# Kernel optimization log

Hardware: AMD Instinct MI355X
Metric: run time of the kernel (lower is better)

Reference implementation:

```python
import jax, jax.numpy as jnp
import numpy as np

N = 100_000   # nodes
E = 3_200_000 # edges (avg degree 32)
F_NODE = 64
F_EDGE = 16
HID = 64
NEG_SLOPE = 0.2


def _gat_conv(x, src, dst, edge_attr, W, a_src, a_dst, We, a_e, bias, n):
    """PyG GATConv (heads=1, edge_dim, add_self_loops=True fill='mean', eval mode)."""
    # --- add self loops; loop edge_attr = mean of incoming edge_attr per node ---
    deg = jax.ops.segment_sum(jnp.ones((src.shape[0],), x.dtype), dst, num_segments=n)
    loop_attr = jax.ops.segment_sum(edge_attr, dst, num_segments=n)
    loop_attr = jnp.where(deg[:, None] > 0, loop_attr / jnp.maximum(deg, 1.0)[:, None], 0.0)
    loop = jnp.arange(n, dtype=src.dtype)
    src2 = jnp.concatenate([src, loop])
    dst2 = jnp.concatenate([dst, loop])
    ea = jnp.concatenate([edge_attr, loop_attr], axis=0)

    # --- node / edge projections and per-node attention terms ---
    h = x @ W                                   # [N, HID]
    alpha_src = h @ a_src                       # [N]
    alpha_dst = h @ a_dst                       # [N]
    e = ea @ We                                 # [E+N, HID]
    alpha_e = e @ a_e                           # [E+N]

    # --- per-edge logits + segment softmax over destination neighborhoods ---
    logits = jax.nn.leaky_relu(alpha_src[src2] + alpha_dst[dst2] + alpha_e, NEG_SLOPE)
    seg_max = jax.ops.segment_max(logits, dst2, num_segments=n)  # every node has self loop
    ex = jnp.exp(logits - seg_max[dst2])
    denom = jax.ops.segment_sum(ex, dst2, num_segments=n)
    w = ex / denom[dst2]                        # [E+N]

    # --- weighted scatter-aggregate of messages ---
    out = jax.ops.segment_sum(h[src2] * w[:, None], dst2, num_segments=n)
    return out + bias


def setup_inputs() -> dict:
    key = jax.random.key(0)
    ks = jax.random.split(key, 16)
    s = 0.1  # keep logits tame
    return {
        "x": jax.random.normal(ks[0], (N, F_NODE), jnp.float32),
        "edge_index": jax.random.randint(ks[1], (2, E), 0, N, jnp.int32),
        "edge_attr": jax.random.normal(ks[2], (E, F_EDGE), jnp.float32),
        "W1": jax.random.normal(ks[3], (F_NODE, HID), jnp.float32) * s,
        "att_src1": jax.random.normal(ks[4], (HID,), jnp.float32) * s,
        "att_dst1": jax.random.normal(ks[5], (HID,), jnp.float32) * s,
        "We1": jax.random.normal(ks[6], (F_EDGE, HID), jnp.float32) * s,
        "att_edge1": jax.random.normal(ks[7], (HID,), jnp.float32) * s,
        "b1": jnp.zeros((HID,), jnp.float32),
        "W2": jax.random.normal(ks[8], (HID, HID), jnp.float32) * s,
        "att_src2": jax.random.normal(ks[9], (HID,), jnp.float32) * s,
        "att_dst2": jax.random.normal(ks[10], (HID,), jnp.float32) * s,
        "We2": jax.random.normal(ks[11], (F_EDGE, HID), jnp.float32) * s,
        "att_edge2": jax.random.normal(ks[12], (HID,), jnp.float32) * s,
        "b2": jnp.zeros((HID,), jnp.float32),
        "fc_w": jax.random.normal(ks[13], (HID, 1), jnp.float32) * s,
        "fc_b": jnp.zeros((1,), jnp.float32),
    }


def reference(x, edge_index, edge_attr, W1, att_src1, att_dst1, We1, att_edge1, b1,
              W2, att_src2, att_dst2, We2, att_edge2, b2, fc_w, fc_b):
    src, dst = edge_index[0], edge_index[1]
    n = x.shape[0]
    h = jax.nn.elu(_gat_conv(x, src, dst, edge_attr, W1, att_src1, att_dst1, We1, att_edge1, b1, n))
    h = jax.nn.elu(_gat_conv(h, src, dst, edge_attr, W2, att_src2, att_dst2, We2, att_edge2, b2, n))
    return h @ fc_w + fc_b  # [N, 1] logits
```

## Files before the change

kernel.cpp:

```cpp
#include <hip/hip_runtime.h>
#include <hip/hip_bf16.h>
#include <hip/hip_fp16.h>
#include <math.h>
#include <stdint.h>

constexpr int HIDDIM = 64;
constexpr int FEDGE  = 16;
constexpr int BN     = 512;
constexpr int CAP    = 17000;
constexpr int TILE   = 4096;
constexpr int NTA    = 512;
constexpr int EPT    = TILE / NTA;
constexpr int GBLK   = 1536;

__global__ void compute_c_kernel(const float* __restrict__ We1, const float* __restrict__ ae1,
                                 const float* __restrict__ We2, const float* __restrict__ ae2,
                                 float* __restrict__ c, int* __restrict__ bucketCursor) {
  int t = threadIdx.x;
  if (t < 512) bucketCursor[t] = 0;
  if (t < FEDGE) {
    float s = 0.f;
    for (int j = 0; j < HIDDIM; ++j) s += We1[t * HIDDIM + j] * ae1[j];
    c[t] = s;
  } else if (t < 2 * FEDGE) {
    int k = t - FEDGE;
    float s = 0.f;
    for (int j = 0; j < HIDDIM; ++j) s += We2[k * HIDDIM + j] * ae2[j];
    c[FEDGE + k] = s;
  }
}

__device__ __forceinline__ int pack_ae(float a1, float a2) {
  unsigned lo = __half_as_ushort(__float2half_rn(a1));
  unsigned hi = __half_as_ushort(__float2half_rn(a2));
  return (int)((hi << 16) | lo);
}
template <int SEL>
__device__ __forceinline__ float unpack_ae(int pk) {
  unsigned u = (SEL == 0) ? ((unsigned)pk & 0xFFFFu) : ((unsigned)pk >> 16);
  return __half2float(__ushort_as_half((unsigned short)u));
}

__global__ __launch_bounds__(NTA) void passA_gemm_kernel(
    const int* __restrict__ src, const int* __restrict__ dst,
    const float* __restrict__ attr, const float* __restrict__ c,
    int* __restrict__ bucketCursor, int2* __restrict__ P, int E, int nbuck, int ablocks,
    const float* __restrict__ X, const float* __restrict__ W,
    const float* __restrict__ a_src, const float* __restrict__ a_dst,
    __half2* __restrict__ H, float* __restrict__ alpha_s, float* __restrict__ alpha_d, int N) {
  __shared__ char smem[57856];
  int t = threadIdx.x;

  if (blockIdx.x < ablocks) {
    int*  st_ae = (int*)smem;
    int*  s_key = st_ae + TILE;
    int*  s_ae  = s_key + TILE;
    unsigned char* s_b = (unsigned char*)(s_ae + TILE);
    int*  cnt   = (int*)(s_b + TILE);
    int*  lbase = cnt + 256;
    int*  gbase = lbase + 512;
    int*  wsum  = gbase + 256;
    float* cs   = (float*)(wsum + 8);

    if (t < 32) cs[t] = c[t];
    if (t < nbuck) cnt[t] = 0;
    __syncthreads();
    int e0 = blockIdx.x * TILE;
    int tileCnt = min(TILE, E - e0);

    int d_reg[EPT];
#pragma unroll
    for (int k = 0; k < EPT; ++k) {
      int e = e0 + k * NTA + t;
      d_reg[k] = (e < E) ? dst[e] : -1;
    }
#pragma unroll
    for (int k = 0; k < EPT; ++k) {
      if (d_reg[k] >= 0) atomicAdd(&cnt[d_reg[k] >> 9], 1);
    }
    __syncthreads();

    int lane = t & 63, w = t >> 6;
    int n = (t < nbuck) ? cnt[t] : 0;
    int ret = 0;
    if (n > 0) ret = atomicAdd(&bucketCursor[t], n);
    int incl = n;
#pragma unroll
    for (int d = 1; d < 64; d <<= 1) {
      int tv = __shfl_up(incl, d, 64);
      if (lane >= d) incl += tv;
    }
    if (lane == 63) wsum[w] = incl;
    __syncthreads();
    {
      int woff = 0;
#pragma unroll
      for (int w2 = 0; w2 < 8; ++w2) woff += (w2 < w) ? wsum[w2] : 0;
      lbase[t] = incl - n + woff;
      if (t < nbuck) { gbase[t] = ret; cnt[t] = 0; }
    }

    {
      int q   = t & 3;
      int grp = t >> 2;
      const float4* attr4 = (const float4*)attr;
#pragma unroll
      for (int pass = 0; pass < TILE / 128; ++pass) {
        int el = pass * 128 + grp;
        int e = e0 + el;
        float4 v = make_float4(0.f, 0.f, 0.f, 0.f);
        if (e < E) v = attr4[(size_t)e * 4 + q];
        float a1 = v.x * cs[4*q]    + v.y * cs[4*q+1]    + v.z * cs[4*q+2]    + v.w * cs[4*q+3];
        float a2 = v.x * cs[16+4*q] + v.y * cs[16+4*q+1] + v.z * cs[16+4*q+2] + v.w * cs[16+4*q+3];
        a1 += __shfl_xor(a1, 1, 64); a1 += __shfl_xor(a1, 2, 64);
        a2 += __shfl_xor(a2, 1, 64); a2 += __shfl_xor(a2, 2, 64);
        if (q == 0) st_ae[el] = pack_ae(a1, a2);
      }
    }
    __syncthreads();

#pragma unroll
    for (int k = 0; k < EPT; ++k) {
      int d = d_reg[k];
      if (d < 0) continue;
      int el = k * NTA + t;
      int e = e0 + el;
      int b = d >> 9;
      int sE = src[e];
      int r = atomicAdd(&cnt[b], 1);
      int idx = lbase[b] + r;
      s_key[idx] = sE | ((d & 511) << 20);
      s_ae[idx]  = st_ae[el];
      s_b[idx]   = (unsigned char)b;
    }
    __syncthreads();

    for (int i = t; i < tileCnt; i += NTA) {
      int b = s_b[i];
      int rank = i - lbase[b];
      int pos = gbase[b] + rank;
      if (pos < CAP) P[(size_t)b * CAP + pos] = make_int2(s_key[i], s_ae[i]);
    }
  } else {
    float* Ws   = (float*)smem;
    float* as_s = Ws + HIDDIM * HIDDIM;
    float* ad_s = as_s + HIDDIM;
    for (int i = t; i < HIDDIM * HIDDIM; i += NTA) Ws[i] = W[i];
    if (t < HIDDIM) {
      as_s[t] = a_src[t];
      ad_s[t] = a_dst[t];
    }
    __syncthreads();
    int lane = t & 63;
    int wid  = t >> 6;
    int gbid = blockIdx.x - ablocks;
    int wavesTotal = 8 * GBLK;
    for (int row = gbid * 8 + wid; row < N; row += wavesTotal) {
      float xv = X[(size_t)row * HIDDIM + lane];
      float acc = 0.f;
#pragma unroll
      for (int k = 0; k < HIDDIM; ++k) {
        float xk = __shfl(xv, k, 64);
        acc = fmaf(xk, Ws[k * HIDDIM + lane], acc);
      }
      float accN = __shfl_xor(acc, 1, 64);
      if (!(lane & 1)) {
        H[(size_t)row * 32 + (lane >> 1)] = __floats2half2_rn(acc, accN);
      }
      float s1 = acc * as_s[lane];
      float s2 = acc * ad_s[lane];
#pragma unroll
      for (int d = 32; d > 0; d >>= 1) {
        s1 += __shfl_xor(s1, d, 64);
        s2 += __shfl_xor(s2, d, 64);
      }
      if (lane == 0) {
        alpha_s[row] = s1;
        alpha_d[row] = s2;
      }
    }
  }
}

__global__ void scan_buckets_kernel(const int* __restrict__ bucketCursor,
                                    int* __restrict__ bucketBase,
                                    int* __restrict__ offsets, int nbuck, int N, int E) {
  __shared__ int s[512];
  int t = threadIdx.x;
  int v = (t < nbuck) ? min(bucketCursor[t], CAP) : 0;
  s[t] = v;
  __syncthreads();
  for (int d = 1; d < 512; d <<= 1) {
    int tv = (t >= d) ? s[t - d] : 0;
    __syncthreads();
    s[t] += tv;
    __syncthreads();
  }
  if (t < nbuck) bucketBase[t] = s[t] - v;
  if (t == 0) offsets[N] = E;
}

__global__ __launch_bounds__(512) void passB_kernel(
    const int2* __restrict__ P, const int* __restrict__ bucketCursor,
    const int* __restrict__ bucketBase, int* __restrict__ offsets,
    int2* __restrict__ EDGS, int N) {
  int b = blockIdx.x;
  int t = threadIdx.x;
  int nodeBase = b * BN;
  int cnt = min(bucketCursor[b], CAP);
  int gbase = bucketBase[b];
  __shared__ int hist[BN];
  __shared__ int cur[BN];
  __shared__ int wsum[8];
  hist[t] = 0;
  __syncthreads();
  const int2* Pb = P + (size_t)b * CAP;
  for (int i = t; i < cnt; i += 512) {
    int dl = (Pb[i].x >> 20) & 511;
    atomicAdd(&hist[dl], 1);
  }
  __syncthreads();
  int deg = hist[t];
  int lane = t & 63, w = t >> 6;
  int incl = deg;
#pragma unroll
  for (int d = 1; d < 64; d <<= 1) {
    int tv = __shfl_up(incl, d, 64);
    if (lane >= d) incl += tv;
  }
  if (lane == 63) wsum[w] = incl;
  __syncthreads();
  int woff = 0;
#pragma unroll
  for (int w2 = 0; w2 < 8; ++w2) woff += (w2 < w) ? wsum[w2] : 0;
  int excl = incl - deg + woff;
  int nodeId = nodeBase + t;
  if (nodeId < N) offsets[nodeId] = gbase + excl;
  cur[t] = gbase + excl;
  __syncthreads();
  for (int i = t; i < cnt; i += 512) {
    int2 r = Pb[i];
    int dl = (r.x >> 20) & 511;
    int pos = atomicAdd(&cur[dl], 1);
    EDGS[pos] = r;
  }
}

template <bool IN16>
__global__ __launch_bounds__(256) void gemm_alpha_kernel(
    const void* __restrict__ Xv, const float* __restrict__ W,
    const float* __restrict__ a_src, const float* __restrict__ a_dst,
    __half2* __restrict__ H, float* __restrict__ alpha_s, float* __restrict__ alpha_d, int n) {
  __shared__ float Ws[HIDDIM * HIDDIM];
  __shared__ float as_s[HIDDIM], ad_s[HIDDIM];
  for (int i = threadIdx.x; i < HIDDIM * HIDDIM; i += blockDim.x) Ws[i] = W[i];
  if (threadIdx.x < HIDDIM) {
    as_s[threadIdx.x] = a_src[threadIdx.x];
    ad_s[threadIdx.x] = a_dst[threadIdx.x];
  }
  __syncthreads();
  int lane = threadIdx.x & 63;
  int wid  = threadIdx.x >> 6;
  int wavesTotal = (blockDim.x >> 6) * gridDim.x;
  for (int row = blockIdx.x * (blockDim.x >> 6) + wid; row < n; row += wavesTotal) {
    float xv;
    if (IN16) xv = __half2float(((const __half*)Xv)[(size_t)row * HIDDIM + lane]);
    else      xv = ((const float*)Xv)[(size_t)row * HIDDIM + lane];
    float acc = 0.f;
#pragma unroll
    for (int k = 0; k < HIDDIM; ++k) {
      float xk = __shfl(xv, k, 64);
      acc = fmaf(xk, Ws[k * HIDDIM + lane], acc);
    }
    float accN = __shfl_xor(acc, 1, 64);
    if (!(lane & 1)) {
      H[(size_t)row * 32 + (lane >> 1)] = __floats2half2_rn(acc, accN);
    }
    float s1 = acc * as_s[lane];
    float s2 = acc * ad_s[lane];
#pragma unroll
    for (int d = 32; d > 0; d >>= 1) {
      s1 += __shfl_xor(s1, d, 64);
      s2 += __shfl_xor(s2, d, 64);
    }
    if (lane == 0) {
      alpha_s[row] = s1;
      alpha_d[row] = s2;
    }
  }
}

__device__ __forceinline__ float leaky(float x) { return (x < 0.f) ? 0.2f * x : x; }
__device__ __forceinline__ float elu(float x) { return (x > 0.f) ? x : (__expf(x) - 1.f); }

template <bool FINAL, int SEL>
__global__ __launch_bounds__(256) void aggregate_kernel(
    const __half2* __restrict__ H, const float* __restrict__ alpha_s, const float* __restrict__ alpha_d,
    const int2* __restrict__ EDGS, const int* __restrict__ offsets,
    const float* __restrict__ bias, const float* __restrict__ fc_w, const float* __restrict__ fc_b,
    void* __restrict__ out, int n) {
  int lane = threadIdx.x & 63;
  int wid  = threadIdx.x >> 6;
  int node = blockIdx.x * (blockDim.x >> 6) + wid;
  if (node >= n) return;
  int off = offsets[node];
  int deg = offsets[node + 1] - off;
  float ad  = alpha_d[node];
  float asn = alpha_s[node];

  if (deg <= 64) {
    int2 ed = make_int2(0, 0);
    if (lane < deg) ed = EDGS[off + lane];
    int   s_l  = ed.x & 0xFFFFF;
    float ae_l = unpack_ae<SEL>(ed.y);
    float as_g = (lane < deg) ? alpha_s[s_l] : 0.f;
    float lg_l = (lane < deg) ? leaky(as_g + ad + ae_l) : -INFINITY;
    float aesum = (lane < deg) ? ae_l : 0.f;
    float lmax = lg_l;
#pragma unroll
    for (int d = 32; d > 0; d >>= 1) {
      lmax = fmaxf(lmax, __shfl_xor(lmax, d, 64));
      aesum += __shfl_xor(aesum, d, 64);
    }
    float self_ae = (deg > 0) ? aesum / (float)deg : 0.f;
    float slg = leaky(asn + ad + self_ae);
    float m = fmaxf(lmax, slg);

    float ex_l = (lane < deg) ? __expf(lg_l - m) : 0.f;
    float dsum = ex_l;
#pragma unroll
    for (int d = 32; d > 0; d >>= 1) dsum += __shfl_xor(dsum, d, 64);
    float exs = __expf(slg - m);
    float denom = dsum + exs;

    int half = lane >> 5;
    int c32  = lane & 31;

    float selfw = (half == 0) ? exs : 0.f;
    float2 hv = __half22float2(H[(size_t)node * 32 + c32]);
    float2 acc2;
    acc2.x = selfw * hv.x;
    acc2.y = selfw * hv.y;

    int jj = 0;
    for (; jj + 16 <= deg; jj += 16) {
      int   si[8]; float ei[8];
#pragma unroll
      for (int k = 0; k < 8; ++k) {
        si[k] = __shfl(s_l, jj + 2 * k + half, 64);
        ei[k] = __shfl(ex_l, jj + 2 * k + half, 64);
      }
      float2 hh[8];
#pragma unroll
      for (int k = 0; k < 8; ++k) hh[k] = __half22float2(H[(size_t)si[k] * 32 + c32]);
#pragma unroll
      for (int k = 0; k < 8; ++k) {
        acc2.x = fmaf(ei[k], hh[k].x, acc2.x);
        acc2.y = fmaf(ei[k], hh[k].y, acc2.y);
      }
    }
    for (; jj + 8 <= deg; jj += 8) {
      int j0 = jj + half, j1 = jj + 2 + half, j2 = jj + 4 + half, j3 = jj + 6 + half;
      int   sa = __shfl(s_l, j0, 64),  sb = __shfl(s_l, j1, 64);
      int   sc = __shfl(s_l, j2, 64),  sd = __shfl(s_l, j3, 64);
      float ea = __shfl(ex_l, j0, 64), eb = __shfl(ex_l, j1, 64);
      float ec = __shfl(ex_l, j2, 64), ef = __shfl(ex_l, j3, 64);
      float2 ha = __half22float2(H[(size_t)sa * 32 + c32]);
      float2 hb = __half22float2(H[(size_t)sb * 32 + c32]);
      float2 hc = __half22float2(H[(size_t)sc * 32 + c32]);
      float2 hd = __half22float2(H[(size_t)sd * 32 + c32]);
      acc2.x = fmaf(ea, ha.x, acc2.x); acc2.y = fmaf(ea, ha.y, acc2.y);
      acc2.x = fmaf(eb, hb.x, acc2.x); acc2.y = fmaf(eb, hb.y, acc2.y);
      acc2.x = fmaf(ec, hc.x, acc2.x); acc2.y = fmaf(ec, hc.y, acc2.y);
      acc2.x = fmaf(ef, hd.x, acc2.x); acc2.y = fmaf(ef, hd.y, acc2.y);
    }
    for (; jj < deg; jj += 2) {
      int j = jj + half;
      int   sj = __shfl(s_l, j, 64);
      float ej = __shfl(ex_l, j, 64);
      float2 hj = __half22float2(H[(size_t)sj * 32 + c32]);
      acc2.x = fmaf(ej, hj.x, acc2.x);
      acc2.y = fmaf(ej, hj.y, acc2.y);
    }
    acc2.x += __shfl_xor(acc2.x, 32, 64);
    acc2.y += __shfl_xor(acc2.y, 32, 64);

    const float2* bi2 = (const float2*)bias;
    float2 bv = bi2[c32];
    float rx = elu(acc2.x / denom + bv.x);
    float ry = elu(acc2.y / denom + bv.y);
    if (!FINAL) {
      if (half == 0) {
        ((__half2*)out)[(size_t)node * 32 + c32] = __floats2half2_rn(rx, ry);
      }
    } else {
      const float2* fw2 = (const float2*)fc_w;
      float2 fv = fw2[c32];
      float s1 = rx * fv.x + ry * fv.y;
#pragma unroll
      for (int d = 16; d > 0; d >>= 1) s1 += __shfl_xor(s1, d, 64);
      if (lane == 0) ((float*)out)[node] = s1 + fc_b[0];
    }
    return;
  }

  {
    const __half* Hh = (const __half*)H;
    float lmax = -INFINITY, aesum = 0.f;
    for (int base = 0; base < deg; base += 64) {
      int i = base + lane;
      if (i < deg) {
        int2 ed = EDGS[off + i];
        int s = ed.x & 0xFFFFF;
        float ae = unpack_ae<SEL>(ed.y);
        float lg = leaky(alpha_s[s] + ad + ae);
        lmax = fmaxf(lmax, lg);
        aesum += ae;
      }
    }
#pragma unroll
    for (int d = 32; d > 0; d >>= 1) {
      lmax = fmaxf(lmax, __shfl_xor(lmax, d, 64));
      aesum += __shfl_xor(aesum, d, 64);
    }
    float self_ae = aesum / (float)deg;
    float slg = leaky(asn + ad + self_ae);
    float m = fmaxf(lmax, slg);
    float exs = __expf(slg - m);
    float dsum = 0.f;
    float acc = exs * __half2float(Hh[(size_t)node * HIDDIM + lane]);
    for (int base = 0; base < deg; base += 64) {
      int i = base + lane;
      int cnt = min(64, deg - base);
      int2 ed = make_int2(0, 0);
      if (i < deg) ed = EDGS[off + i];
      int   s_l  = ed.x & 0xFFFFF;
      float ae_l = unpack_ae<SEL>(ed.y);
      float ex_l = (lane < cnt) ? __expf(leaky(alpha_s[s_l] + ad + ae_l) - m) : 0.f;
      dsum += ex_l;
      for (int j = 0; j < cnt; ++j) {
        int   sj = __shfl(s_l, j, 64);
        float ej = __shfl(ex_l, j, 64);
        acc = fmaf(ej, __half2float(Hh[(size_t)sj * HIDDIM + lane]), acc);
      }
    }
#pragma unroll
    for (int d = 32; d > 0; d >>= 1) dsum += __shfl_xor(dsum, d, 64);
    float denom = dsum + exs;

    float res = elu(acc / denom + bias[lane]);
    if (!FINAL) {
      ((__half*)out)[(size_t)node * HIDDIM + lane] = __float2half_rn(res);
    } else {
      float s1 = res * fc_w[lane];
#pragma unroll
      for (int d = 32; d > 0; d >>= 1) s1 += __shfl_xor(s1, d, 64);
      if (lane == 0) ((float*)out)[node] = s1 + fc_b[0];
    }
  }
}

extern "C" void kernel_launch(void* const* d_in, const int* in_sizes, int n_in,
                              void* d_out, int out_size, void* d_ws, size_t ws_size,
                              hipStream_t stream) {
  const float* x    = (const float*)d_in[0];
  const int*   ei   = (const int*)d_in[1];
  const float* attr = (const float*)d_in[2];
  const float* W1   = (const float*)d_in[3];
  const float* as1  = (const float*)d_in[4];
  const float* ad1  = (const float*)d_in[5];
  const float* We1  = (const float*)d_in[6];
  const float* ae1  = (const float*)d_in[7];
  const float* b1   = (const float*)d_in[8];
  const float* W2   = (const float*)d_in[9];
  const float* as2  = (const float*)d_in[10];
  const float* ad2  = (const float*)d_in[11];
  const float* We2  = (const float*)d_in[12];
  const float* ae2  = (const float*)d_in[13];
  const float* b2   = (const float*)d_in[14];
  const float* fcw  = (const float*)d_in[15];
  const float* fcb  = (const float*)d_in[16];

  const int N = in_sizes[0] / HIDDIM;
  const int E = in_sizes[1] / 2;
  const int NBUCK = (N + BN - 1) / BN;

  char* p = (char*)d_ws;
  auto alloc = [&](size_t bytes) -> void* {
    void* r = (void*)p;
    p += (bytes + 255) & ~(size_t)255;
    return r;
  };
  float*  c            = (float*)alloc(32 * sizeof(float));
  int*    bucketCursor = (int*)alloc(512 * 4);
  int*    bucketBase   = (int*)alloc(((size_t)NBUCK + 1) * 4);
  int*    offsets      = (int*)alloc(((size_t)N + 1) * 4);
  float*  alpha_s      = (float*)alloc((size_t)N * 4);
  float*  alpha_d      = (float*)alloc((size_t)N * 4);
  int2*   EDGS         = (int2*)alloc((size_t)E * 8);
  int2*   P            = (int2*)alloc((size_t)NBUCK * CAP * 8);
  __half2* H           = (__half2*)alloc((size_t)N * 32 * 4);
  __half2* X2          = (__half2*)alloc((size_t)N * 32 * 4);

  const int* srcp = ei;
  const int* dstp = ei + E;

  compute_c_kernel<<<1, 512, 0, stream>>>(We1, ae1, We2, ae2, c, bucketCursor);

  int ablocks = (E + TILE - 1) / TILE;
  passA_gemm_kernel<<<ablocks + GBLK, NTA, 0, stream>>>(
      srcp, dstp, attr, c, bucketCursor, P, E, NBUCK, ablocks,
      x, W1, as1, ad1, H, alpha_s, alpha_d, N);

  scan_buckets_kernel<<<1, 512, 0, stream>>>(bucketCursor, bucketBase, offsets, NBUCK, N, E);
  passB_kernel<<<NBUCK, 512, 0, stream>>>(P, bucketCursor, bucketBase, offsets, EDGS, N);

  int aggBlocks = (N + 3) / 4;

  aggregate_kernel<false, 0><<<aggBlocks, 256, 0, stream>>>(H, alpha_s, alpha_d, EDGS,
                                                            offsets, b1, nullptr, nullptr, X2, N);
  gemm_alpha_kernel<true><<<2048, 256, 0, stream>>>(X2, W2, as2, ad2, H, alpha_s, alpha_d, N);
  aggregate_kernel<true, 1><<<aggBlocks, 256, 0, stream>>>(H, alpha_s, alpha_d, EDGS,
                                                           offsets, b2, fcw, fcb, d_out, N);
}
```

Baseline: 431.9 us.

## Fold bucket scan into passB and halve passA edge tile size

Removes the single-block bucket scan kernel. Every passB block now redoes the prefix sum over bucket counts with wave shuffles and picks its own base offset, which saves a launch and a serial dependency at the cost of redundant work in each block. The passA edge tile also drops from 4096 to 2048 with matching shared memory, giving more blocks and lower LDS use per block, but more atomics on the global bucket cursors.

Measured after the change: 450.3 us. +4.3%, slower.

```diff
diff --git a/kernel.cpp b/kernel.cpp
--- a/kernel.cpp
+++ b/kernel.cpp
@@ -8,7 +8,7 @@
 constexpr int FEDGE  = 16;
 constexpr int BN     = 512;
 constexpr int CAP    = 17000;
-constexpr int TILE   = 4096;
+constexpr int TILE   = 2048;
 constexpr int NTA    = 512;
 constexpr int EPT    = TILE / NTA;
 constexpr int GBLK   = 1536;
@@ -48,7 +48,7 @@
     const float* __restrict__ X, const float* __restrict__ W,
     const float* __restrict__ a_src, const float* __restrict__ a_dst,
     __half2* __restrict__ H, float* __restrict__ alpha_s, float* __restrict__ alpha_d, int N) {
-  __shared__ char smem[57856];
+  __shared__ char smem[30912];
   int t = threadIdx.x;
 
   if (blockIdx.x < ablocks) {
@@ -182,38 +182,41 @@
   }
 }
 
-__global__ void scan_buckets_kernel(const int* __restrict__ bucketCursor,
-                                    int* __restrict__ bucketBase,
-                                    int* __restrict__ offsets, int nbuck, int N, int E) {
-  __shared__ int s[512];
-  int t = threadIdx.x;
-  int v = (t < nbuck) ? min(bucketCursor[t], CAP) : 0;
-  s[t] = v;
-  __syncthreads();
-  for (int d = 1; d < 512; d <<= 1) {
-    int tv = (t >= d) ? s[t - d] : 0;
-    __syncthreads();
-    s[t] += tv;
-    __syncthreads();
-  }
-  if (t < nbuck) bucketBase[t] = s[t] - v;
-  if (t == 0) offsets[N] = E;
-}
-
 __global__ __launch_bounds__(512) void passB_kernel(
     const int2* __restrict__ P, const int* __restrict__ bucketCursor,
-    const int* __restrict__ bucketBase, int* __restrict__ offsets,
-    int2* __restrict__ EDGS, int N) {
+    int* __restrict__ offsets, int2* __restrict__ EDGS, int nbuck, int N, int E) {
   int b = blockIdx.x;
   int t = threadIdx.x;
   int nodeBase = b * BN;
-  int cnt = min(bucketCursor[b], CAP);
-  int gbase = bucketBase[b];
   __shared__ int hist[BN];
   __shared__ int cur[BN];
   __shared__ int wsum[8];
-  hist[t] = 0;
+  __shared__ int gbase_sh;
+
+  int lane = t & 63, w = t >> 6;
+  {
+    int v = (t < nbuck) ? min(bucketCursor[t], CAP) : 0;
+    int incl = v;
+#pragma unroll
+    for (int d = 1; d < 64; d <<= 1) {
+      int tv = __shfl_up(incl, d, 64);
+      if (lane >= d) incl += tv;
+    }
+    if (lane == 63) wsum[w] = incl;
+    hist[t] = 0;
+    if (t + 512 < BN) hist[t + 512] = 0;
+    __syncthreads();
+    int woff = 0;
+#pragma unroll
+    for (int w2 = 0; w2 < 8; ++w2) woff += (w2 < w) ? wsum[w2] : 0;
+    int excl = incl - v + woff;
+    if (t == b) gbase_sh = excl;
+    if (b == 0 && t == 0) offsets[N] = E;
+  }
   __syncthreads();
+  int gbase = gbase_sh;
+  int cnt = min(bucketCursor[b], CAP);
+
   const int2* Pb = P + (size_t)b * CAP;
   for (int i = t; i < cnt; i += 512) {
     int dl = (Pb[i].x >> 20) & 511;
@@ -221,7 +224,6 @@
   }
   __syncthreads();
   int deg = hist[t];
-  int lane = t & 63, w = t >> 6;
   int incl = deg;
 #pragma unroll
   for (int d = 1; d < 64; d <<= 1) {
@@ -493,7 +495,6 @@
   };
   float*  c            = (float*)alloc(32 * sizeof(float));
   int*    bucketCursor = (int*)alloc(512 * 4);
-  int*    bucketBase   = (int*)alloc(((size_t)NBUCK + 1) * 4);
   int*    offsets      = (int*)alloc(((size_t)N + 1) * 4);
   float*  alpha_s      = (float*)alloc((size_t)N * 4);
   float*  alpha_d      = (float*)alloc((size_t)N * 4);
@@ -512,8 +513,7 @@
       srcp, dstp, attr, c, bucketCursor, P, E, NBUCK, ablocks,
       x, W1, as1, ad1, H, alpha_s, alpha_d, N);
 
-  scan_buckets_kernel<<<1, 512, 0, stream>>>(bucketCursor, bucketBase, offsets, NBUCK, N, E);
-  passB_kernel<<<NBUCK, 512, 0, stream>>>(P, bucketCursor, bucketBase, offsets, EDGS, N);
+  passB_kernel<<<NBUCK, 512, 0, stream>>>(P, bucketCursor, offsets, EDGS, NBUCK, N, E);
 
   int aggBlocks = (N + 3) / 4;
 
```
